# Kernel optimization log

Measured on AMD Instinct MI355X. Metric: run time of the kernel, lower is better.

The kernel has to match this reference:

```python
import jax, jax.numpy as jnp
import numpy as np
from jax import lax

B, CIN, LIN = 65536, 1, 274
D, S, H, NL = 16, 18, 4, 4
DH = D // H  # 4
HID = 64
EPS = 1e-5

def layer_norm(x, g, b):
    m = jnp.mean(x, axis=-1, keepdims=True)
    v = jnp.mean(jnp.square(x - m), axis=-1, keepdims=True)
    return (x - m) * lax.rsqrt(v + EPS) * g + b

def setup_inputs() -> dict:
    key = jax.random.key(0)
    ks = jax.random.split(key, 16)
    n = lambda k, shp, s=0.05: jax.random.normal(k, shp, dtype=jnp.float32) * s
    return {
        "x": jax.random.normal(ks[0], (B, CIN, LIN), dtype=jnp.float32),
        "patch_w": n(ks[1], (D, CIN, 16), 0.2),   # Conv1d weight (O,I,K)
        "patch_b": jnp.zeros((D,), jnp.float32),
        "pos_embed": n(ks[2], (1, S, D), 0.02),
        "ln1_g": jnp.ones((NL, D), jnp.float32),
        "ln1_b": jnp.zeros((NL, D), jnp.float32),
        "qkv_w": n(ks[3], (NL, 3 * D, D), 0.2),    # in_proj_weight per layer
        "qkv_b": jnp.zeros((NL, 3 * D), jnp.float32),
        "out_w": n(ks[4], (NL, D, D), 0.2),
        "out_b": jnp.zeros((NL, D), jnp.float32),
        "ln2_g": jnp.ones((NL, D), jnp.float32),
        "ln2_b": jnp.zeros((NL, D), jnp.float32),
        "mlp_w1": n(ks[5], (NL, HID, D), 0.2),
        "mlp_b1": jnp.zeros((NL, HID), jnp.float32),
        "mlp_w2": n(ks[6], (NL, D, HID), 0.2),
        "mlp_b2": jnp.zeros((NL, D), jnp.float32),
        "lnf_g": jnp.ones((D,), jnp.float32),
        "lnf_b": jnp.zeros((D,), jnp.float32),
        "dec_w": n(ks[7], (D, CIN, 16), 0.2),      # ConvTranspose1d weight (I,O,K)
        "dec_b": jnp.zeros((CIN,), jnp.float32),
    }

def reference(x, patch_w, patch_b, pos_embed, ln1_g, ln1_b, qkv_w, qkv_b,
              out_w, out_b, ln2_g, ln2_b, mlp_w1, mlp_b1, mlp_w2, mlp_b2,
              lnf_g, lnf_b, dec_w, dec_b):
    dn = ('NCH', 'OIH', 'NCH')
    # patchify: (B,1,274) -> (B,16,18) -> (B,18,16)
    h = lax.conv_general_dilated(x, patch_w, (16,), [(7, 7)], dimension_numbers=dn)
    h = h + patch_b[None, :, None]
    h = jnp.transpose(h, (0, 2, 1)) + pos_embed
    scale = 1.0 / np.sqrt(DH)
    for i in range(NL):
        xn = layer_norm(h, ln1_g[i], ln1_b[i])
        qkv = xn @ qkv_w[i].T + qkv_b[i]                      # (B,S,3D)
        q, k, v = jnp.split(qkv, 3, axis=-1)
        q = q.reshape(B, S, H, DH)
        k = k.reshape(B, S, H, DH)
        v = v.reshape(B, S, H, DH)
        att = jnp.einsum('bqhd,bkhd->bhqk', q, k) * scale
        att = jax.nn.softmax(att, axis=-1)
        o = jnp.einsum('bhqk,bkhd->bqhd', att, v).reshape(B, S, D)
        h = h + (o @ out_w[i].T + out_b[i])
        xn2 = layer_norm(h, ln2_g[i], ln2_b[i])
        m = jax.nn.gelu(xn2 @ mlp_w1[i].T + mlp_b1[i], approximate=False)
        h = h + (m @ mlp_w2[i].T + mlp_b2[i])
    h = layer_norm(h, lnf_g, lnf_b)
    z = jnp.transpose(h, (0, 2, 1))                            # (B,16,18)
    # ConvTranspose1d(k=16, s=16, p=7): lhs_dilation=16, pad=k-1-p=8, flipped kernel
    w_t = jnp.transpose(jnp.flip(dec_w, axis=-1), (1, 0, 2))   # (O=1, I=16, 16)
    out = lax.conv_general_dilated(z, w_t, (1,), [(8, 8)], lhs_dilation=(16,),
                                   dimension_numbers=dn)
    out = out + dec_b[None, :, None]                            # (B,1,274)
    return out, z
```

## Files before the change

kernel.cpp:

```cpp
#include <hip/hip_runtime.h>
#include <math.h>
#include <stdint.h>

#define NB      65536
#define LIN     274
#define SEQ     18
#define DM      16
#define NH      4
#define HID     64
#define NLAYER  4
#define EPSF    1e-5f

#define EPB      8
#define NTHREADS 192
#define SMEM_F32 2688
#define VT_BYTE_OFF 4608

#define QS 0.72134752044448170f

typedef _Float16 h2    __attribute__((ext_vector_type(2)));
typedef _Float16 f16x4 __attribute__((ext_vector_type(4)));
typedef _Float16 f16x8 __attribute__((ext_vector_type(8)));
typedef float    f32x4 __attribute__((ext_vector_type(4)));
typedef __fp16   hf2_raw __attribute__((ext_vector_type(2)));

#if __has_builtin(__builtin_amdgcn_fdot2)
__device__ __forceinline__ float fdot2(h2 a, h2 b, float c) { return __builtin_amdgcn_fdot2(a, b, c, false); }
#else
__device__ __forceinline__ float fdot2(h2 a, h2 b, float c) { return c + (float)a[0] * (float)b[0] + (float)a[1] * (float)b[1]; }
#endif
#if __has_builtin(__builtin_amdgcn_cvt_pkrtz)
__device__ __forceinline__ h2 pkrtz(float a, float b) {
    hf2_raw r = __builtin_amdgcn_cvt_pkrtz(a, b);
    return __builtin_bit_cast(h2, r);
}
#else
__device__ __forceinline__ h2 pkrtz(float a, float b) { h2 r; r[0] = (_Float16)a; r[1] = (_Float16)b; return r; }
#endif

#if __has_builtin(__builtin_amdgcn_mfma_f32_16x16x16f16)
__device__ __forceinline__ f32x4 MFMA16(f16x4 a, f16x4 b, f32x4 c) {
    return __builtin_amdgcn_mfma_f32_16x16x16f16(a, b, c, 0, 0, 0);
}
#elif __has_builtin(__builtin_amdgcn_mfma_f32_16x16x16_f16)
__device__ __forceinline__ f32x4 MFMA16(f16x4 a, f16x4 b, f32x4 c) {
    return __builtin_amdgcn_mfma_f32_16x16x16_f16(a, b, c, 0, 0, 0);
}
#else
__device__ __forceinline__ f32x4 MFMA16(f16x4 a, f16x4 b, f32x4 c) {
    f32x4 d;
    asm volatile("v_mfma_f32_16x16x16_f16 %0, %1, %2, %3"
                 : "=v"(d) : "v"(a), "v"(b), "v"(c));
    return d;
}
#endif

__device__ __forceinline__ float fast_rcp(float x)  { return __builtin_amdgcn_rcpf(x); }
__device__ __forceinline__ float fast_rsq(float x)  { return __builtin_amdgcn_rsqf(x); }
__device__ __forceinline__ float fast_exp2(float x) { return __builtin_amdgcn_exp2f(x); }

__device__ __forceinline__ float gelu_tanh(float t) {
    const float A2 = 0.79788456080286536f * 2.88539008177792681f;
    const float B2 = 0.03567740814183430f * 2.88539008177792681f;
    float u  = t * fmaf(t * t, B2, A2);
    float e  = fast_exp2(u);
    float r  = fast_rcp(e + 1.0f);
    return fmaf(-t, r, t);
}

__device__ __forceinline__ f16x4 pk4(float a, float b, float c, float d) {
    h2 lo = pkrtz(a, b), hi = pkrtz(c, d);
    f16x4 r; r[0] = lo[0]; r[1] = lo[1]; r[2] = hi[0]; r[3] = hi[1];
    return r;
}
__device__ __forceinline__ f32x4 ld4(const float* p) {
    float4 t = *(const float4*)p;
    f32x4 r; r[0] = t.x; r[1] = t.y; r[2] = t.z; r[3] = t.w;
    return r;
}
__device__ __forceinline__ h2 h2at(f16x8 v, int i) {
    h2 r; r[0] = v[2 * i]; r[1] = v[2 * i + 1]; return r;
}

#define WS_H2_COUNT 6400
#define WS_BIAS_FLOATS (NLAYER * 112)
#define WS_TOTAL_BYTES (WS_H2_COUNT * 4 + WS_BIAS_FLOATS * 4)
#define PREP_ITEMS (WS_H2_COUNT + WS_BIAS_FLOATS)

__global__ __launch_bounds__(512) void prep_weights(
    const float* __restrict__ patch_w, const float* __restrict__ dec_w,
    const float* __restrict__ qkv_w, const float* __restrict__ out_w,
    const float* __restrict__ mlp_w1, const float* __restrict__ mlp_w2,
    const float* __restrict__ ln1_g, const float* __restrict__ ln1_b,
    const float* __restrict__ ln2_g, const float* __restrict__ ln2_b,
    const float* __restrict__ qkv_b, const float* __restrict__ mlp_b1,
    h2* __restrict__ ws)
{
    int i = blockIdx.x * 512 + threadIdx.x;
    if (i >= PREP_ITEMS) return;
    if (i < WS_H2_COUNT) {
        int tile = i >> 7;
        int lane = (i >> 1) & 63;
        int p    = i & 1;
        int row  = lane & 15;
        int kb   = (lane >> 4) * 4 + 2 * p;
        float a, b;
        if (tile == 0)      { a = patch_w[row * 16 + kb];  b = patch_w[row * 16 + kb + 1]; }
        else if (tile == 1) { a = dec_w[kb * 16 + row];    b = dec_w[(kb + 1) * 16 + row]; }
        else {
            int t2 = tile - 2, li = t2 / 12, j = t2 % 12;
            const float* s;
            float g0 = 1.0f, g1v = 1.0f;
            if (j < 3) {
                s = qkv_w + li * 768 + (j * 16 + row) * 16 + kb;
                g0 = ln1_g[li * 16 + kb]; g1v = ln1_g[li * 16 + kb + 1];
                if (j == 0) { g0 *= QS; g1v *= QS; }
            } else if (j == 3) {
                s = out_w + li * 256 + row * 16 + kb;
            } else if (j < 8) {
                s = mlp_w1 + li * 1024 + ((j - 4) * 16 + row) * 16 + kb;
                g0 = ln2_g[li * 16 + kb]; g1v = ln2_g[li * 16 + kb + 1];
            } else {
                s = mlp_w2 + li * 1024 + row * 64 + (j - 8) * 16 + kb;
            }
            a = s[0] * g0; b = s[1] * g1v;
        }
        ws[i] = pkrtz(a, b);
    } else {
        int t = i - WS_H2_COUNT;
        int li = t / 112, r = t % 112;
        float* wbf = (float*)(ws + WS_H2_COUNT);
        float bv;
        if (r < 48) {
            const float* Wr = qkv_w + li * 768 + r * 16;
            const float* lb = ln1_b + li * 16;
            bv = qkv_b[li * 48 + r];
            for (int d = 0; d < 16; ++d) bv = fmaf(Wr[d], lb[d], bv);
            if (r < 16) bv *= QS;
        } else {
            int j = r - 48;
            const float* Wr = mlp_w1 + li * 1024 + j * 16;
            const float* lb = ln2_b + li * 16;
            bv = mlp_b1[li * 64 + j];
            for (int d = 0; d < 16; ++d) bv = fmaf(Wr[d], lb[d], bv);
        }
        wbf[li * 112 + r] = bv;
    }
}

__global__ __launch_bounds__(NTHREADS) void ae_fwd(
    const float* __restrict__ x,
    const float* __restrict__ patch_b, const float* __restrict__ pos_embed,
    const h2*    __restrict__ wp, const float* __restrict__ wb,
    const float* __restrict__ out_b, const float* __restrict__ mlp_b2,
    const float* __restrict__ lnf_g, const float* __restrict__ lnf_b,
    const float* __restrict__ dec_b,
    float* __restrict__ out_y, float* __restrict__ out_z)
{
    __shared__ float smem[SMEM_F32];
    const int tid  = threadIdx.x;
    const int lane = tid & 63;
    const int wv   = tid >> 6;
    const int col  = lane & 15;
    const int g16  = lane >> 4;
    const int fb   = g16 * 4;

    {
        const float4* xg = (const float4*)(x + (long long)blockIdx.x * (EPB * LIN));
        float4* xs = (float4*)smem;
        for (int i = tid; i < (EPB * LIN) / 4; i += NTHREADS) xs[i] = xg[i];
    }
    __syncthreads();

    int elemL[3], sIdx[3];
    #pragma unroll
    for (int t = 0; t < 3; ++t) {
        int T = wv * 48 + t * 16 + col;
        int e = (T * 57) >> 10;
        elemL[t] = e;
        sIdx[t]  = T - 18 * e;
    }

    const f16x4* wfrag = (const f16x4*)wp;
    const f16x4 wpatch = wfrag[lane];
    const f16x4 wdec   = wfrag[64 + lane];
    h2 ones2; ones2[0] = (_Float16)1.0f; ones2[1] = (_Float16)1.0f;

    float hacc[3][4];
    {
        const float4 pb = *(const float4*)(patch_b + fb);
        #pragma unroll
        for (int t = 0; t < 3; ++t) {
            float xv[4];
            #pragma unroll
            for (int r = 0; r < 4; ++r) {
                int loc = sIdx[t] * 16 - 7 + fb + r;
                xv[r] = (loc >= 0 && loc < LIN) ? smem[elemL[t] * LIN + loc] : 0.0f;
            }
            f16x4 xb = pk4(xv[0], xv[1], xv[2], xv[3]);
            const float4 pe = *(const float4*)(pos_embed + sIdx[t] * DM + fb);
            f32x4 c; c[0] = pb.x + pe.x; c[1] = pb.y + pe.y; c[2] = pb.z + pe.z; c[3] = pb.w + pe.w;
            c = MFMA16(wpatch, xb, c);
            #pragma unroll
            for (int r = 0; r < 4; ++r) hacc[t][r] = c[r];
        }
    }

    #pragma unroll 1
    for (int li = 0; li < NLAYER; ++li) {
        const f16x4* wl = wfrag + (2 + li * 12) * 64 + lane;
        const float* wbL = wb + li * 112;
        const f32x4 bq = ld4(wbL + fb);
        const f32x4 bk = ld4(wbL + 16 + fb);
        const f32x4 bv = ld4(wbL + 32 + fb);
        f32x4 b1r[4];
        #pragma unroll
        for (int c = 0; c < 4; ++c) b1r[c] = ld4(wbL + 48 + c * 16 + fb);
        const float4 ob4 = *(const float4*)(out_b + li * DM + fb);
        const f32x4 b2r = ld4(mlp_b2 + li * DM + fb);

        h2 qp[3][2]; f16x4 kpk[3], vpk[3];
        #pragma unroll
        for (int t = 0; t < 3; ++t) {
            float a0 = hacc[t][0], a1 = hacc[t][1], a2 = hacc[t][2], a3 = hacc[t][3];
            float sm = a0 + a1 + a2 + a3;
            float qq = fmaf(a0, a0, fmaf(a1, a1, fmaf(a2, a2, a3 * a3)));
            sm += __shfl_xor(sm, 16); sm += __shfl_xor(sm, 32);
            qq += __shfl_xor(qq, 16); qq += __shfl_xor(qq, 32);
            float mean = sm * (1.0f / 16.0f);
            float var  = fmaxf(fmaf(mean, -mean, qq * (1.0f / 16.0f)), 0.0f);
            float inv  = fast_rsq(var + EPSF);
            float mi   = mean * inv;
            f16x4 xb = pk4(fmaf(a0, inv, -mi), fmaf(a1, inv, -mi),
                           fmaf(a2, inv, -mi), fmaf(a3, inv, -mi));
            f32x4 aq = MFMA16(wl[0],   xb, bq);
            f32x4 ak = MFMA16(wl[64],  xb, bk);
            f32x4 av = MFMA16(wl[128], xb, bv);
            qp[t][0] = pkrtz(aq[0], aq[1]);
            qp[t][1] = pkrtz(aq[2], aq[3]);
            kpk[t] = pk4(ak[0], ak[1], ak[2], ak[3]);
            vpk[t] = pk4(av[0], av[1], av[2], av[3]);
        }
        __syncthreads();
        #pragma unroll
        for (int t = 0; t < 3; ++t) {
            ((f16x4*)smem)[(elemL[t] * 4 + g16) * 18 + sIdx[t]] = kpk[t];
            _Float16* vt = (_Float16*)((char*)smem + VT_BYTE_OFF) + elemL[t] * 384 + g16 * 24 + sIdx[t];
            vt[0]   = vpk[t][0];
            vt[96]  = vpk[t][1];
            vt[192] = vpk[t][2];
            vt[288] = vpk[t][3];
        }
        __syncthreads();

        #pragma unroll
        for (int t = 0; t < 3; ++t) {
            const char* Kb = (const char*)smem + (elemL[t] * 4 + g16) * 144;
            const char* Vb = (const char*)smem + VT_BYTE_OFF + elemL[t] * 768 + g16 * 48;
            h2 w9[9];
            #pragma unroll
            for (int jp = 0; jp < 9; ++jp) {
                f16x8 k2 = *(const f16x8*)(Kb + jp * 16);
                float s0 = fdot2(qp[t][1], h2at(k2, 1), fdot2(qp[t][0], h2at(k2, 0), 0.0f));
                float s1 = fdot2(qp[t][1], h2at(k2, 3), fdot2(qp[t][0], h2at(k2, 2), 0.0f));
                w9[jp] = pkrtz(fast_exp2(s0), fast_exp2(s1));
            }
            float sA = 0.0f, sB = 0.0f;
            #pragma unroll
            for (int jp = 0; jp < 8; jp += 2) {
                sA = fdot2(w9[jp], ones2, sA);
                sB = fdot2(w9[jp + 1], ones2, sB);
            }
            sA = fdot2(w9[8], ones2, sA);
            float inv = fast_rcp(sA + sB);
            float o[4];
            #pragma unroll
            for (int d = 0; d < 4; ++d) {
                const char* vr = Vb + d * 192;
                f16x8 v8a = *(const f16x8*)vr;
                f16x8 v8b = *(const f16x8*)(vr + 16);
                h2 vtl = *(const h2*)(vr + 32);
                float acc = fdot2(w9[8], vtl, 0.0f);
                #pragma unroll
                for (int jp = 0; jp < 4; ++jp) acc = fdot2(w9[jp], h2at(v8a, jp), acc);
                #pragma unroll
                for (int jp = 0; jp < 4; ++jp) acc = fdot2(w9[4 + jp], h2at(v8b, jp), acc);
                o[d] = acc * inv;
            }
            f16x4 obf = pk4(o[0], o[1], o[2], o[3]);
            f32x4 oa; oa[0] = ob4.x; oa[1] = ob4.y; oa[2] = ob4.z; oa[3] = ob4.w;
            oa = MFMA16(wl[192], obf, oa);
            #pragma unroll
            for (int r = 0; r < 4; ++r) hacc[t][r] += oa[r];
        }

        #pragma unroll
        for (int t = 0; t < 3; ++t) {
            float a0 = hacc[t][0], a1 = hacc[t][1], a2 = hacc[t][2], a3 = hacc[t][3];
            float sm = a0 + a1 + a2 + a3;
            float qq = fmaf(a0, a0, fmaf(a1, a1, fmaf(a2, a2, a3 * a3)));
            sm += __shfl_xor(sm, 16); sm += __shfl_xor(sm, 32);
            qq += __shfl_xor(qq, 16); qq += __shfl_xor(qq, 32);
            float mean = sm * (1.0f / 16.0f);
            float var  = fmaxf(fmaf(mean, -mean, qq * (1.0f / 16.0f)), 0.0f);
            float inv  = fast_rsq(var + EPSF);
            float mi   = mean * inv;
            f16x4 xb2 = pk4(fmaf(a0, inv, -mi), fmaf(a1, inv, -mi),
                            fmaf(a2, inv, -mi), fmaf(a3, inv, -mi));
            f32x4 acc2 = b2r;
            #pragma unroll
            for (int c = 0; c < 4; ++c) {
                f32x4 m1 = MFMA16(wl[(4 + c) * 64], xb2, b1r[c]);
                f16x4 gb = pk4(gelu_tanh(m1[0]), gelu_tanh(m1[1]),
                               gelu_tanh(m1[2]), gelu_tanh(m1[3]));
                acc2 = MFMA16(wl[(8 + c) * 64], gb, acc2);
            }
            #pragma unroll
            for (int r = 0; r < 4; ++r) hacc[t][r] += acc2[r];
        }
    }

    const float4 gf = *(const float4*)(lnf_g + fb);
    const float4 bf = *(const float4*)(lnf_b + fb);
    const float db0 = dec_b[0];
    #pragma unroll
    for (int t = 0; t < 3; ++t) {
        float a0 = hacc[t][0], a1 = hacc[t][1], a2 = hacc[t][2], a3 = hacc[t][3];
        float sm = a0 + a1 + a2 + a3;
        float qq = fmaf(a0, a0, fmaf(a1, a1, fmaf(a2, a2, a3 * a3)));
        sm += __shfl_xor(sm, 16); sm += __shfl_xor(sm, 32);
        qq += __shfl_xor(qq, 16); qq += __shfl_xor(qq, 32);
        float mean = sm * (1.0f / 16.0f);
        float var  = fmaxf(fmaf(mean, -mean, qq * (1.0f / 16.0f)), 0.0f);
        float inv  = fast_rsq(var + EPSF);
        float mi   = mean * inv;
        float f0 = fmaf(fmaf(a0, inv, -mi), gf.x, bf.x);
        float f1 = fmaf(fmaf(a1, inv, -mi), gf.y, bf.y);
        float f2 = fmaf(fmaf(a2, inv, -mi), gf.z, bf.z);
        float f3 = fmaf(fmaf(a3, inv, -mi), gf.w, bf.w);

        long long eg = (long long)blockIdx.x * EPB + elemL[t];
        float* zb = out_z + eg * (DM * SEQ) + sIdx[t];
        zb[(fb + 0) * SEQ] = f0; zb[(fb + 1) * SEQ] = f1;
        zb[(fb + 2) * SEQ] = f2; zb[(fb + 3) * SEQ] = f3;

        f16x4 hb = pk4(f0, f1, f2, f3);
        f32x4 y4 = {0.f, 0.f, 0.f, 0.f};
        y4 = MFMA16(wdec, hb, y4);
        float* yb = out_y + eg * LIN;
        int p0 = sIdx[t] * 16 + fb - 7;
        #pragma unroll
        for (int r = 0; r < 4; ++r) {
            int p = p0 + r;
            if (p >= 0 && p < LIN) yb[p] = y4[r] + db0;
        }
    }
}

#define EPB_F 14
#define NT_F  252
__global__ __launch_bounds__(NT_F) void ae_fwd_f32(
    const float* __restrict__ x,
    const float* __restrict__ patch_w, const float* __restrict__ patch_b,
    const float* __restrict__ pos_embed,
    const float* __restrict__ ln1_g, const float* __restrict__ ln1_b,
    const float* __restrict__ qkv_w, const float* __restrict__ qkv_b,
    const float* __restrict__ out_w, const float* __restrict__ out_b,
    const float* __restrict__ ln2_g, const float* __restrict__ ln2_b,
    const float* __restrict__ mlp_w1, const float* __restrict__ mlp_b1,
    const float* __restrict__ mlp_w2, const float* __restrict__ mlp_b2,
    const float* __restrict__ lnf_g, const float* __restrict__ lnf_b,
    const float* __restrict__ dec_w, const float* __restrict__ dec_b,
    float* __restrict__ out_y, float* __restrict__ out_z)
{
    __shared__ float s_kv[EPB_F * 580];
    const int tid = threadIdx.x;
    const int e   = tid / SEQ;
    const int s   = tid - e * SEQ;
    const long long b = (long long)blockIdx.x * EPB_F + e;
    const bool valid = (b < NB);
    {
        const long long base = (long long)blockIdx.x * (EPB_F * LIN);
        const long long lim  = (long long)NB * LIN - 1;
        for (int i = tid; i < EPB_F * LIN; i += NT_F) {
            long long gi = base + i;
            if (gi > lim) gi = lim;
            s_kv[i] = x[gi];
        }
    }
    __syncthreads();
    float xv[16];
    {
        const float* xe = &s_kv[e * LIN];
        #pragma unroll
        for (int k = 0; k < 16; ++k) {
            int idx = s * 16 - 7 + k;
            xv[k] = (idx >= 0 && idx < LIN) ? xe[idx] : 0.0f;
        }
    }
    float h[DM];
    #pragma unroll
    for (int d = 0; d < DM; ++d) {
        float acc = patch_b[d] + pos_embed[s * DM + d];
        #pragma unroll
        for (int k = 0; k < 16; ++k) acc = fmaf(xv[k], patch_w[d * 16 + k], acc);
        h[d] = acc;
    }
    #pragma unroll 1
    for (int li = 0; li < NLAYER; ++li) {
        float xn[DM];
        {
            float m = 0.f;
            #pragma unroll
            for (int d = 0; d < DM; ++d) m += h[d];
            m *= (1.0f / DM);
            float v = 0.f;
            #pragma unroll
            for (int d = 0; d < DM; ++d) { float t = h[d] - m; v = fmaf(t, t, v); }
            v *= (1.0f / DM);
            float inv = fast_rsq(v + EPSF);
            #pragma unroll
            for (int d = 0; d < DM; ++d) xn[d] = (h[d] - m) * inv * ln1_g[li * DM + d] + ln1_b[li * DM + d];
        }
        float q[DM], kk[DM], vv[DM];
        {
            const float* W  = qkv_w + li * 48 * DM;
            const float* Wb = qkv_b + li * 48;
            #pragma unroll
            for (int j = 0; j < DM; ++j) {
                float aq = Wb[j], ak = Wb[DM + j], av = Wb[2 * DM + j];
                #pragma unroll
                for (int d = 0; d < DM; ++d) {
                    float xd = xn[d];
                    aq = fmaf(xd, W[j * DM + d], aq);
                    ak = fmaf(xd, W[(DM + j) * DM + d], ak);
                    av = fmaf(xd, W[(2 * DM + j) * DM + d], av);
                }
                q[j] = aq; kk[j] = ak; vv[j] = av;
            }
        }
        __syncthreads();
        {
            float* kb = &s_kv[e * 580];
            float* vb = kb + SEQ * DM;
            #pragma unroll
            for (int j = 0; j < DM; ++j) kb[s * DM + j] = kk[j];
            #pragma unroll
            for (int j = 0; j < DM; ++j) vb[s * DM + j] = vv[j];
        }
        __syncthreads();
        float o[DM];
        {
            const float* kb = &s_kv[e * 580];
            const float* vb = kb + SEQ * DM;
            #pragma unroll
            for (int hh = 0; hh < NH; ++hh) {
                const float qscale = 0.5f * 1.44269504088896341f;
                const float q0 = q[hh * 4] * qscale, q1 = q[hh * 4 + 1] * qscale;
                const float q2 = q[hh * 4 + 2] * qscale, q3 = q[hh * 4 + 3] * qscale;
                float sc[SEQ];
                float ssum = 0.f;
                #pragma unroll
                for (int j = 0; j < SEQ; ++j) {
                    const float4 kj = *(const float4*)(kb + j * DM + hh * 4);
                    float t = fmaf(q0, kj.x, fmaf(q1, kj.y, fmaf(q2, kj.z, q3 * kj.w)));
                    float w = fast_exp2(t);
                    sc[j] = w; ssum += w;
                }
                const float inv = fast_rcp(ssum);
                float a0 = 0.f, a1 = 0.f, a2 = 0.f, a3 = 0.f;
                #pragma unroll
                for (int j = 0; j < SEQ; ++j) {
                    const float4 vj = *(const float4*)(vb + j * DM + hh * 4);
                    const float w = sc[j] * inv;
                    a0 = fmaf(w, vj.x, a0); a1 = fmaf(w, vj.y, a1);
                    a2 = fmaf(w, vj.z, a2); a3 = fmaf(w, vj.w, a3);
                }
                o[hh * 4] = a0; o[hh * 4 + 1] = a1; o[hh * 4 + 2] = a2; o[hh * 4 + 3] = a3;
            }
        }
        {
            const float* W  = out_w + li * DM * DM;
            #pragma unroll
            for (int d = 0; d < DM; ++d) {
                float acc = out_b[li * DM + d];
                #pragma unroll
                for (int d2 = 0; d2 < DM; ++d2) acc = fmaf(o[d2], W[d * DM + d2], acc);
                h[d] += acc;
            }
        }
        float xn2[DM];
        {
            float m = 0.f;
            #pragma unroll
            for (int d = 0; d < DM; ++d) m += h[d];
            m *= (1.0f / DM);
            float v = 0.f;
            #pragma unroll
            for (int d = 0; d < DM; ++d) { float t = h[d] - m; v = fmaf(t, t, v); }
            v *= (1.0f / DM);
            float inv = fast_rsq(v + EPSF);
            #pragma unroll
            for (int d = 0; d < DM; ++d) xn2[d] = (h[d] - m) * inv * ln2_g[li * DM + d] + ln2_b[li * DM + d];
        }
        {
            const float* W1 = mlp_w1 + li * HID * DM;
            const float* W2 = mlp_w2 + li * DM * HID;
            float acc2[DM];
            #pragma unroll
            for (int d = 0; d < DM; ++d) acc2[d] = mlp_b2[li * DM + d];
            #pragma unroll 2
            for (int j = 0; j < HID; ++j) {
                float t = mlp_b1[li * HID + j];
                #pragma unroll
                for (int d = 0; d < DM; ++d) t = fmaf(xn2[d], W1[j * DM + d], t);
                float g = gelu_tanh(t);
                #pragma unroll
                for (int d = 0; d < DM; ++d) acc2[d] = fmaf(g, W2[d * HID + j], acc2[d]);
            }
            #pragma unroll
            for (int d = 0; d < DM; ++d) h[d] += acc2[d];
        }
    }
    {
        float m = 0.f;
        #pragma unroll
        for (int d = 0; d < DM; ++d) m += h[d];
        m *= (1.0f / DM);
        float v = 0.f;
        #pragma unroll
        for (int d = 0; d < DM; ++d) { float t = h[d] - m; v = fmaf(t, t, v); }
        v *= (1.0f / DM);
        float inv = fast_rsq(v + EPSF);
        #pragma unroll
        for (int d = 0; d < DM; ++d) h[d] = (h[d] - m) * inv * lnf_g[d] + lnf_b[d];
    }
    if (valid) {
        float* zb = out_z + b * (DM * SEQ);
        #pragma unroll
        for (int d = 0; d < DM; ++d) zb[d * SEQ + s] = h[d];
        float* yb = out_y + b * LIN;
        const float db0 = dec_b[0];
        #pragma unroll
        for (int k = 0; k < 16; ++k) {
            int t = s * 16 + k - 7;
            if (t >= 0 && t < LIN) {
                float acc = db0;
                #pragma unroll
                for (int d = 0; d < DM; ++d) acc = fmaf(h[d], dec_w[d * 16 + k], acc);
                yb[t] = acc;
            }
        }
    }
}

extern "C" void kernel_launch(void* const* d_in, const int* in_sizes, int n_in,
                              void* d_out, int out_size, void* d_ws, size_t ws_size,
                              hipStream_t stream) {
    const float* x        = (const float*)d_in[0];
    const float* patch_w  = (const float*)d_in[1];
    const float* patch_b  = (const float*)d_in[2];
    const float* pos_e    = (const float*)d_in[3];
    const float* ln1_g    = (const float*)d_in[4];
    const float* ln1_b    = (const float*)d_in[5];
    const float* qkv_w    = (const float*)d_in[6];
    const float* qkv_b    = (const float*)d_in[7];
    const float* out_w    = (const float*)d_in[8];
    const float* out_b    = (const float*)d_in[9];
    const float* ln2_g    = (const float*)d_in[10];
    const float* ln2_b    = (const float*)d_in[11];
    const float* mlp_w1   = (const float*)d_in[12];
    const float* mlp_b1   = (const float*)d_in[13];
    const float* mlp_w2   = (const float*)d_in[14];
    const float* mlp_b2   = (const float*)d_in[15];
    const float* lnf_g    = (const float*)d_in[16];
    const float* lnf_b    = (const float*)d_in[17];
    const float* dec_w    = (const float*)d_in[18];
    const float* dec_b    = (const float*)d_in[19];

    float* out_y = (float*)d_out;
    float* out_z = out_y + (long long)NB * LIN;

    if (ws_size >= WS_TOTAL_BYTES) {
        h2* wsp = (h2*)d_ws;
        const float* wbp = (const float*)(wsp + WS_H2_COUNT);
        prep_weights<<<(PREP_ITEMS + 511) / 512, 512, 0, stream>>>(
            patch_w, dec_w, qkv_w, out_w, mlp_w1, mlp_w2,
            ln1_g, ln1_b, ln2_g, ln2_b, qkv_b, mlp_b1, wsp);
        ae_fwd<<<NB / EPB, NTHREADS, 0, stream>>>(
            x, patch_b, pos_e, wsp, wbp,
            out_b, mlp_b2, lnf_g, lnf_b, dec_b, out_y, out_z);
    } else {
        const int grid = (NB + EPB_F - 1) / EPB_F;
        ae_fwd_f32<<<grid, NT_F, 0, stream>>>(
            x, patch_w, patch_b, pos_e, ln1_g, ln1_b, qkv_w, qkv_b,
            out_w, out_b, ln2_g, ln2_b, mlp_w1, mlp_b1, mlp_w2, mlp_b2,
            lnf_g, lnf_b, dec_w, dec_b, out_y, out_z);
    }
}
```

Before: 490.7 us.

## Double-buffer K/V shared memory, keep V in fp32, use permlane reductions

Gives shared memory two ping-pong buffers indexed by layer parity, which removes one of the two __syncthreads per layer. V is now stored untransposed in fp32 with a padded stride and read as float4, and the attention weights stay in fp32 with a scalar-FMA weighted sum instead of packed fp16 dot products. LayerNorm cross-lane reductions use permlane16/32 swap builtins when the compiler provides them. The decoder bias is folded into the MFMA accumulator. The cost is more LDS per block, which may lower occupancy, and more VALU work in the PV accumulation.

```diff
diff --git a/kernel.cpp b/kernel.cpp
--- a/kernel.cpp
+++ b/kernel.cpp
@@ -13,8 +13,10 @@
 
 #define EPB      8
 #define NTHREADS 192
-#define SMEM_F32 2688
-#define VT_BYTE_OFF 4608
+#define BUF_DW   3488
+#define VOFF_DW  1152
+#define VSTR     292
+#define SMEM_DW  (2 * BUF_DW)
 
 #define QS 0.72134752044448170f
 
@@ -58,6 +60,21 @@
 __device__ __forceinline__ float fast_rcp(float x)  { return __builtin_amdgcn_rcpf(x); }
 __device__ __forceinline__ float fast_rsq(float x)  { return __builtin_amdgcn_rsqf(x); }
 __device__ __forceinline__ float fast_exp2(float x) { return __builtin_amdgcn_exp2f(x); }
+
+__device__ __forceinline__ float bfly16_32(float x) {
+#if __has_builtin(__builtin_amdgcn_permlane16_swap) && __has_builtin(__builtin_amdgcn_permlane32_swap)
+    unsigned u = __builtin_bit_cast(unsigned, x);
+    auto p16 = __builtin_amdgcn_permlane16_swap(u, u, false, false);
+    float s = __builtin_bit_cast(float, (unsigned)p16[0]) + __builtin_bit_cast(float, (unsigned)p16[1]);
+    unsigned v = __builtin_bit_cast(unsigned, s);
+    auto p32 = __builtin_amdgcn_permlane32_swap(v, v, false, false);
+    return __builtin_bit_cast(float, (unsigned)p32[0]) + __builtin_bit_cast(float, (unsigned)p32[1]);
+#else
+    x += __shfl_xor(x, 16);
+    x += __shfl_xor(x, 32);
+    return x;
+#endif
+}
 
 __device__ __forceinline__ float gelu_tanh(float t) {
     const float A2 = 0.79788456080286536f * 2.88539008177792681f;
@@ -157,7 +174,7 @@
     const float* __restrict__ dec_b,
     float* __restrict__ out_y, float* __restrict__ out_z)
 {
-    __shared__ float smem[SMEM_F32];
+    __shared__ float smem[SMEM_DW];
     const int tid  = threadIdx.x;
     const int lane = tid & 63;
     const int wv   = tid >> 6;
@@ -167,7 +184,7 @@
 
     {
         const float4* xg = (const float4*)(x + (long long)blockIdx.x * (EPB * LIN));
-        float4* xs = (float4*)smem;
+        float4* xs = (float4*)(smem + BUF_DW);
         for (int i = tid; i < (EPB * LIN) / 4; i += NTHREADS) xs[i] = xg[i];
     }
     __syncthreads();
@@ -184,18 +201,18 @@
     const f16x4* wfrag = (const f16x4*)wp;
     const f16x4 wpatch = wfrag[lane];
     const f16x4 wdec   = wfrag[64 + lane];
-    h2 ones2; ones2[0] = (_Float16)1.0f; ones2[1] = (_Float16)1.0f;
 
     float hacc[3][4];
     {
         const float4 pb = *(const float4*)(patch_b + fb);
+        const float* xst = smem + BUF_DW;
         #pragma unroll
         for (int t = 0; t < 3; ++t) {
             float xv[4];
             #pragma unroll
             for (int r = 0; r < 4; ++r) {
                 int loc = sIdx[t] * 16 - 7 + fb + r;
-                xv[r] = (loc >= 0 && loc < LIN) ? smem[elemL[t] * LIN + loc] : 0.0f;
+                xv[r] = (loc >= 0 && loc < LIN) ? xst[elemL[t] * LIN + loc] : 0.0f;
             }
             f16x4 xb = pk4(xv[0], xv[1], xv[2], xv[3]);
             const float4 pe = *(const float4*)(pos_embed + sIdx[t] * DM + fb);
@@ -208,25 +225,24 @@
 
     #pragma unroll 1
     for (int li = 0; li < NLAYER; ++li) {
+        const int bufO = (li & 1) ? BUF_DW : 0;
         const f16x4* wl = wfrag + (2 + li * 12) * 64 + lane;
         const float* wbL = wb + li * 112;
         const f32x4 bq = ld4(wbL + fb);
         const f32x4 bk = ld4(wbL + 16 + fb);
-        const f32x4 bv = ld4(wbL + 32 + fb);
+        const f32x4 bvx = ld4(wbL + 32 + fb);
         f32x4 b1r[4];
         #pragma unroll
         for (int c = 0; c < 4; ++c) b1r[c] = ld4(wbL + 48 + c * 16 + fb);
         const float4 ob4 = *(const float4*)(out_b + li * DM + fb);
         const f32x4 b2r = ld4(mlp_b2 + li * DM + fb);
 
-        h2 qp[3][2]; f16x4 kpk[3], vpk[3];
+        h2 qp[3][2]; f16x4 kpk[3]; f32x4 vreg[3];
         #pragma unroll
         for (int t = 0; t < 3; ++t) {
             float a0 = hacc[t][0], a1 = hacc[t][1], a2 = hacc[t][2], a3 = hacc[t][3];
-            float sm = a0 + a1 + a2 + a3;
-            float qq = fmaf(a0, a0, fmaf(a1, a1, fmaf(a2, a2, a3 * a3)));
-            sm += __shfl_xor(sm, 16); sm += __shfl_xor(sm, 32);
-            qq += __shfl_xor(qq, 16); qq += __shfl_xor(qq, 32);
+            float sm = bfly16_32(a0 + a1 + a2 + a3);
+            float qq = bfly16_32(fmaf(a0, a0, fmaf(a1, a1, fmaf(a2, a2, a3 * a3))));
             float mean = sm * (1.0f / 16.0f);
             float var  = fmaxf(fmaf(mean, -mean, qq * (1.0f / 16.0f)), 0.0f);
             float inv  = fast_rsq(var + EPSF);
@@ -235,59 +251,45 @@
                            fmaf(a2, inv, -mi), fmaf(a3, inv, -mi));
             f32x4 aq = MFMA16(wl[0],   xb, bq);
             f32x4 ak = MFMA16(wl[64],  xb, bk);
-            f32x4 av = MFMA16(wl[128], xb, bv);
+            f32x4 av = MFMA16(wl[128], xb, bvx);
             qp[t][0] = pkrtz(aq[0], aq[1]);
             qp[t][1] = pkrtz(aq[2], aq[3]);
             kpk[t] = pk4(ak[0], ak[1], ak[2], ak[3]);
-            vpk[t] = pk4(av[0], av[1], av[2], av[3]);
+            vreg[t] = av;
+        }
+        #pragma unroll
+        for (int t = 0; t < 3; ++t) {
+            ((f16x4*)(smem + bufO))[(elemL[t] * 4 + g16) * 18 + sIdx[t]] = kpk[t];
+            float4 vv; vv.x = vreg[t][0]; vv.y = vreg[t][1]; vv.z = vreg[t][2]; vv.w = vreg[t][3];
+            *(float4*)(smem + bufO + VOFF_DW + elemL[t] * VSTR + sIdx[t] * 16 + g16 * 4) = vv;
         }
         __syncthreads();
+
         #pragma unroll
         for (int t = 0; t < 3; ++t) {
-            ((f16x4*)smem)[(elemL[t] * 4 + g16) * 18 + sIdx[t]] = kpk[t];
-            _Float16* vt = (_Float16*)((char*)smem + VT_BYTE_OFF) + elemL[t] * 384 + g16 * 24 + sIdx[t];
-            vt[0]   = vpk[t][0];
-            vt[96]  = vpk[t][1];
-            vt[192] = vpk[t][2];
-            vt[288] = vpk[t][3];
-        }
-        __syncthreads();
-
-        #pragma unroll
-        for (int t = 0; t < 3; ++t) {
-            const char* Kb = (const char*)smem + (elemL[t] * 4 + g16) * 144;
-            const char* Vb = (const char*)smem + VT_BYTE_OFF + elemL[t] * 768 + g16 * 48;
-            h2 w9[9];
+            const int e = elemL[t];
+            const f16x4* Kb = (const f16x4*)(smem + bufO) + (e * 4 + g16) * 18;
+            float sc[SEQ]; float ssum = 0.0f;
             #pragma unroll
             for (int jp = 0; jp < 9; ++jp) {
-                f16x8 k2 = *(const f16x8*)(Kb + jp * 16);
+                f16x8 k2 = *(const f16x8*)(Kb + 2 * jp);
                 float s0 = fdot2(qp[t][1], h2at(k2, 1), fdot2(qp[t][0], h2at(k2, 0), 0.0f));
                 float s1 = fdot2(qp[t][1], h2at(k2, 3), fdot2(qp[t][0], h2at(k2, 2), 0.0f));
-                w9[jp] = pkrtz(fast_exp2(s0), fast_exp2(s1));
-            }
-            float sA = 0.0f, sB = 0.0f;
-            #pragma unroll
-            for (int jp = 0; jp < 8; jp += 2) {
-                sA = fdot2(w9[jp], ones2, sA);
-                sB = fdot2(w9[jp + 1], ones2, sB);
-            }
-            sA = fdot2(w9[8], ones2, sA);
-            float inv = fast_rcp(sA + sB);
-            float o[4];
-            #pragma unroll
-            for (int d = 0; d < 4; ++d) {
-                const char* vr = Vb + d * 192;
-                f16x8 v8a = *(const f16x8*)vr;
-                f16x8 v8b = *(const f16x8*)(vr + 16);
-                h2 vtl = *(const h2*)(vr + 32);
-                float acc = fdot2(w9[8], vtl, 0.0f);
-                #pragma unroll
-                for (int jp = 0; jp < 4; ++jp) acc = fdot2(w9[jp], h2at(v8a, jp), acc);
-                #pragma unroll
-                for (int jp = 0; jp < 4; ++jp) acc = fdot2(w9[4 + jp], h2at(v8b, jp), acc);
-                o[d] = acc * inv;
-            }
-            f16x4 obf = pk4(o[0], o[1], o[2], o[3]);
+                float w0 = fast_exp2(s0), w1 = fast_exp2(s1);
+                sc[2 * jp] = w0; sc[2 * jp + 1] = w1;
+                ssum += w0 + w1;
+            }
+            float inv = fast_rcp(ssum);
+            const float* vb = smem + bufO + VOFF_DW + e * VSTR + g16 * 4;
+            float o0 = 0.f, o1 = 0.f, o2 = 0.f, o3 = 0.f;
+            #pragma unroll
+            for (int j = 0; j < SEQ; ++j) {
+                float4 vj = *(const float4*)(vb + j * 16);
+                float w = sc[j];
+                o0 = fmaf(w, vj.x, o0); o1 = fmaf(w, vj.y, o1);
+                o2 = fmaf(w, vj.z, o2); o3 = fmaf(w, vj.w, o3);
+            }
+            f16x4 obf = pk4(o0 * inv, o1 * inv, o2 * inv, o3 * inv);
             f32x4 oa; oa[0] = ob4.x; oa[1] = ob4.y; oa[2] = ob4.z; oa[3] = ob4.w;
             oa = MFMA16(wl[192], obf, oa);
             #pragma unroll
@@ -297,10 +299,8 @@
         #pragma unroll
         for (int t = 0; t < 3; ++t) {
             float a0 = hacc[t][0], a1 = hacc[t][1], a2 = hacc[t][2], a3 = hacc[t][3];
-            float sm = a0 + a1 + a2 + a3;
-            float qq = fmaf(a0, a0, fmaf(a1, a1, fmaf(a2, a2, a3 * a3)));
-            sm += __shfl_xor(sm, 16); sm += __shfl_xor(sm, 32);
-            qq += __shfl_xor(qq, 16); qq += __shfl_xor(qq, 32);
+            float sm = bfly16_32(a0 + a1 + a2 + a3);
+            float qq = bfly16_32(fmaf(a0, a0, fmaf(a1, a1, fmaf(a2, a2, a3 * a3))));
             float mean = sm * (1.0f / 16.0f);
             float var  = fmaxf(fmaf(mean, -mean, qq * (1.0f / 16.0f)), 0.0f);
             float inv  = fast_rsq(var + EPSF);
@@ -326,10 +326,8 @@
     #pragma unroll
     for (int t = 0; t < 3; ++t) {
         float a0 = hacc[t][0], a1 = hacc[t][1], a2 = hacc[t][2], a3 = hacc[t][3];
-        float sm = a0 + a1 + a2 + a3;
-        float qq = fmaf(a0, a0, fmaf(a1, a1, fmaf(a2, a2, a3 * a3)));
-        sm += __shfl_xor(sm, 16); sm += __shfl_xor(sm, 32);
-        qq += __shfl_xor(qq, 16); qq += __shfl_xor(qq, 32);
+        float sm = bfly16_32(a0 + a1 + a2 + a3);
+        float qq = bfly16_32(fmaf(a0, a0, fmaf(a1, a1, fmaf(a2, a2, a3 * a3))));
         float mean = sm * (1.0f / 16.0f);
         float var  = fmaxf(fmaf(mean, -mean, qq * (1.0f / 16.0f)), 0.0f);
         float inv  = fast_rsq(var + EPSF);
@@ -345,14 +343,14 @@
         zb[(fb + 2) * SEQ] = f2; zb[(fb + 3) * SEQ] = f3;
 
         f16x4 hb = pk4(f0, f1, f2, f3);
-        f32x4 y4 = {0.f, 0.f, 0.f, 0.f};
+        f32x4 y4; y4[0] = db0; y4[1] = db0; y4[2] = db0; y4[3] = db0;
         y4 = MFMA16(wdec, hb, y4);
         float* yb = out_y + eg * LIN;
         int p0 = sIdx[t] * 16 + fb - 7;
         #pragma unroll
         for (int r = 0; r < 4; ++r) {
             int p = p0 + r;
-            if (p >= 0 && p < LIN) yb[p] = y4[r] + db0;
+            if (p >= 0 && p < LIN) yb[p] = y4[r];
         }
     }
 }
```

Result: no change. 492.7 us (+0.4%).
